# Kernel optimization log

Hardware: AMD Instinct MI355X
Metric: run time of the kernel (lower is better)

Reference implementation:

```python
import jax, jax.numpy as jnp
import numpy as np

LATENT = 64

def _linear(x, W, b):
    return x @ W.T + b

def setup_inputs() -> dict:
    key = jax.random.key(0)
    ks = jax.random.split(key, 16)
    B, D, H, L = 16384, 784, 1024, LATENT
    def u(k, shape, fan_in):
        bound = 1.0 / np.sqrt(fan_in)
        return jax.random.uniform(k, shape, jnp.float32, -bound, bound)
    inp = {
        "x": jax.random.uniform(ks[0], (B, D), jnp.float32),
        "epsilon": jax.random.normal(ks[1], (B, L), jnp.float32),
        "W_ih": u(ks[2], (H, D), D), "b_ih": u(ks[3], (H,), D),
        "W_m":  u(ks[4], (L, H), H), "b_m":  u(ks[5], (L,), H),
        "W_lv": u(ks[6], (L, H), H), "b_lv": u(ks[7], (L,), H),
        "W_ap": u(ks[8], (L, H), H), "b_ap": u(ks[9], (L,), H),
        "W_lh": u(ks[10], (H, L), L), "b_lh": u(ks[11], (H,), L),
        "W_ho": u(ks[12], (D, H), H), "b_ho": u(ks[13], (D,), H),
    }
    return inp

def reference(x, epsilon, W_ih, b_ih, W_m, b_m, W_lv, b_lv, W_ap, b_ap, W_lh, b_lh, W_ho, b_ho):
    # ----- encode -----
    hidden = jnp.tanh(_linear(x, W_ih, b_ih))            # [B,H]
    mean   = _linear(hidden, W_m, b_m)                   # [B,L]
    logvar = jnp.clip(_linear(hidden, W_lv, b_lv), -4.5, 0.0)  # Hardtanh(-4.5,0)
    approx = _linear(hidden, W_ap, b_ap)                 # [B,L]
    # ----- reparameterize (rank-1 Gaussian) -----
    # inv_cov = diag(exp(logvar)) + approx approx^T   per sample
    B, L = mean.shape
    eye = jnp.eye(L, dtype=mean.dtype)
    inv_cov = jnp.exp(logvar)[:, :, None] * eye + approx[:, :, None] * approx[:, None, :]  # [B,L,L]
    cov = jnp.linalg.inv(inv_cov)                        # batched 64x64 inverse
    # torch.potrf default returns UPPER Cholesky U with U^T U = cov -> U = chol(cov).T
    Sigma = jnp.swapaxes(jnp.linalg.cholesky(cov), -1, -2)  # [B,L,L] upper
    z = mean + jnp.einsum('bij,bj->bi', Sigma, epsilon)  # [B,L]
    # ----- decode -----
    h2 = jnp.tanh(_linear(z, W_lh, b_lh))
    x_mean = jax.nn.sigmoid(_linear(h2, W_ho, b_ho))     # [B,784]
    return (x_mean, z, mean, logvar, approx)
```

## Files before the change

kernel.cpp:

```cpp
#include <hip/hip_runtime.h>
#include <hip/hip_bf16.h>
#include <math.h>

typedef __attribute__((ext_vector_type(8))) short short8;
typedef __attribute__((ext_vector_type(4))) float f32x4;
typedef __attribute__((ext_vector_type(4))) unsigned short us4;

#define GLOBAL_AS __attribute__((address_space(1)))
#define LDS_AS __attribute__((address_space(3)))

__device__ inline void g2l16(const void* g, void* l) {
    __builtin_amdgcn_global_load_lds((const GLOBAL_AS void*)g, (LDS_AS void*)l, 16, 0, 0);
}

__device__ inline unsigned short f2bf(float f) {
    unsigned int u = __float_as_uint(f);
    return (unsigned short)((u + 0x7fffu + ((u >> 16) & 1u)) >> 16);
}

template <int EPI>
__global__ __launch_bounds__(512, 4) void mgemmB(
    const __hip_bfloat16* __restrict__ A,
    const __hip_bfloat16* __restrict__ W,
    const float* __restrict__ bias,
    void* __restrict__ outp,
    int lda, int ldb, int nT, int ldc, int Nreal)
{
    __shared__ __align__(16) __hip_bfloat16 sh[2][12288];

    const int tid  = threadIdx.x;
    const int wave = tid >> 6;
    const int lane = tid & 63;
    const int rBase = blockIdx.x * 256;
    const int cBase = blockIdx.y * 128;

    const __hip_bfloat16* Ab = A + (size_t)rBase * lda;
    const __hip_bfloat16* Wb = W + (size_t)cBase * ldb;

    const int wr = (wave >> 1) * 64;
    const int wc = (wave & 1) * 64;
    const int h  = lane >> 4;
    const int r0 = lane & 15;
    const int swz = h ^ ((r0 >> 1) & 3);

    f32x4 acc[4][4];
#pragma unroll
    for (int m = 0; m < 4; ++m)
#pragma unroll
        for (int n = 0; n < 4; ++n) acc[m][n] = (f32x4){0.f, 0.f, 0.f, 0.f};

    auto stage = [&](int bb, int t) {
        const int k0 = t * 32;
#pragma unroll
        for (int r = 0; r < 2; ++r) {
            int s2  = r * 512 + tid;
            int row = s2 >> 2;
            int cg  = (s2 & 3) ^ ((row >> 1) & 3);
            g2l16(Ab + (size_t)row * lda + k0 + cg * 8, &sh[bb][s2 * 8]);
        }
        {
            int s2  = tid;
            int row = s2 >> 2;
            int cg  = (s2 & 3) ^ ((row >> 1) & 3);
            g2l16(Wb + (size_t)row * ldb + k0 + cg * 8, &sh[bb][8192 + s2 * 8]);
        }
    };

    auto compute = [&](int bb) {
        const __hip_bfloat16* base = &sh[bb][0];
        short8 a_[4], b_[4];
#pragma unroll
        for (int m = 0; m < 4; ++m) {
            int R = wr + m * 16 + r0;
            a_[m] = *(const short8*)(base + (R * 4 + swz) * 8);
        }
#pragma unroll
        for (int n = 0; n < 4; ++n) {
            int R = wc + n * 16 + r0;
            b_[n] = *(const short8*)(base + 8192 + (R * 4 + swz) * 8);
        }
        __builtin_amdgcn_s_setprio(1);
#pragma unroll
        for (int m = 0; m < 4; ++m)
#pragma unroll
            for (int n = 0; n < 4; ++n)
                acc[m][n] = __builtin_amdgcn_mfma_f32_16x16x32_bf16(a_[m], b_[n], acc[m][n], 0, 0, 0);
        __builtin_amdgcn_s_setprio(0);
    };

    stage(0, 0);
    stage(1, 1);
    for (int t = 0; t < nT; ++t) {
        const int cur = t & 1;
        if (t + 1 < nT) asm volatile("s_waitcnt vmcnt(3)" ::: "memory");
        else            asm volatile("s_waitcnt vmcnt(0)" ::: "memory");
        __builtin_amdgcn_s_barrier();
        compute(cur);
        __builtin_amdgcn_s_barrier();
        if (t + 2 < nT) stage(cur, t + 2);
    }

    const int rq = lane >> 4;
    const int c0 = lane & 15;
#pragma unroll
    for (int m = 0; m < 4; ++m) {
#pragma unroll
        for (int n = 0; n < 4; ++n) {
            f32x4 v = acc[m][n];
            const int gc = cBase + wc + n * 16 + c0;
            const float bv = bias[gc];
#pragma unroll
            for (int j = 0; j < 4; ++j) {
                const int gr = rBase + wr + m * 16 + rq * 4 + j;
                float val = v[j] + bv;
                if (EPI == 1) {
                    ((__hip_bfloat16*)outp)[(size_t)gr * ldc + gc] = __float2bfloat16(tanhf(val));
                } else {
                    if (gc < Nreal)
                        ((float*)outp)[(size_t)gr * Nreal + gc] = 1.f / (1.f + expf(-val));
                }
            }
        }
    }
}

template <int EPI>
__global__ __launch_bounds__(256, 4) void mgemmC(
    const __hip_bfloat16* __restrict__ A,
    const __hip_bfloat16* __restrict__ W,
    const float* __restrict__ bias,
    void* __restrict__ outp,
    int lda, int ldb, int nT, int ldc, int Nreal)
{
    __shared__ __align__(16) __hip_bfloat16 sh[2][8192];

    const int tid  = threadIdx.x;
    const int wave = tid >> 6;
    const int lane = tid & 63;
    const int rBase = blockIdx.x * 128;
    const int cBase = blockIdx.y * 128;

    const __hip_bfloat16* Ab = A + (size_t)rBase * lda;
    const __hip_bfloat16* Wb = W + (size_t)cBase * ldb;

    const int wr = (wave >> 1) * 64;
    const int wc = (wave & 1) * 64;
    const int h  = lane >> 4;
    const int r0 = lane & 15;
    const int swz = h ^ ((r0 >> 1) & 3);

    f32x4 acc[4][4];
#pragma unroll
    for (int m = 0; m < 4; ++m)
#pragma unroll
        for (int n = 0; n < 4; ++n) acc[m][n] = (f32x4){0.f, 0.f, 0.f, 0.f};

    auto stage = [&](int bb, int t) {
        const int k0 = t * 32;
#pragma unroll
        for (int r = 0; r < 2; ++r) {
            int s2  = r * 256 + tid;
            int row = s2 >> 2;
            int cg  = (s2 & 3) ^ ((row >> 1) & 3);
            g2l16(Ab + (size_t)row * lda + k0 + cg * 8, &sh[bb][s2 * 8]);
            g2l16(Wb + (size_t)row * ldb + k0 + cg * 8, &sh[bb][4096 + s2 * 8]);
        }
    };

    auto compute = [&](int bb) {
        const __hip_bfloat16* base = &sh[bb][0];
        short8 a_[4], b_[4];
#pragma unroll
        for (int m = 0; m < 4; ++m) {
            int R = wr + m * 16 + r0;
            a_[m] = *(const short8*)(base + (R * 4 + swz) * 8);
        }
#pragma unroll
        for (int n = 0; n < 4; ++n) {
            int R = wc + n * 16 + r0;
            b_[n] = *(const short8*)(base + 4096 + (R * 4 + swz) * 8);
        }
        __builtin_amdgcn_s_setprio(1);
#pragma unroll
        for (int m = 0; m < 4; ++m)
#pragma unroll
            for (int n = 0; n < 4; ++n)
                acc[m][n] = __builtin_amdgcn_mfma_f32_16x16x32_bf16(a_[m], b_[n], acc[m][n], 0, 0, 0);
        __builtin_amdgcn_s_setprio(0);
    };

    stage(0, 0);
    stage(1, 1);
    for (int t = 0; t < nT; ++t) {
        const int cur = t & 1;
        if (t + 1 < nT) asm volatile("s_waitcnt vmcnt(4)" ::: "memory");
        else            asm volatile("s_waitcnt vmcnt(0)" ::: "memory");
        __builtin_amdgcn_s_barrier();
        compute(cur);
        __builtin_amdgcn_s_barrier();
        if (t + 2 < nT) stage(cur, t + 2);
    }

    const int rq = lane >> 4;
    const int c0 = lane & 15;
#pragma unroll
    for (int m = 0; m < 4; ++m) {
#pragma unroll
        for (int n = 0; n < 4; ++n) {
            f32x4 v = acc[m][n];
            const int gc = cBase + wc + n * 16 + c0;
            const float bv = bias[gc];
#pragma unroll
            for (int j = 0; j < 4; ++j) {
                const int gr = rBase + wr + m * 16 + rq * 4 + j;
                float val = v[j] + bv;
                if (EPI == 1) {
                    ((__hip_bfloat16*)outp)[(size_t)gr * ldc + gc] = __float2bfloat16(tanhf(val));
                }
            }
        }
    }
}

__global__ __launch_bounds__(256, 2) void headrep(
    const __hip_bfloat16* __restrict__ hidden,
    const __hip_bfloat16* __restrict__ Whead,
    const float* __restrict__ bhead,
    const float* __restrict__ eps,
    float* __restrict__ meanp, float* __restrict__ logvarp,
    float* __restrict__ approxp, float* __restrict__ zp,
    __hip_bfloat16* __restrict__ zb)
{
    __shared__ __align__(16) __hip_bfloat16 sh[2][16384];

    const int tid  = threadIdx.x;
    const int wave = tid >> 6;
    const int lane = tid & 63;
    const int rBase = blockIdx.x * 64;

    const __hip_bfloat16* Ab = hidden + (size_t)rBase * 1024;

    const int wnb = wave * 48;
    const int h  = lane >> 4;
    const int r0 = lane & 15;
    const int swz = h ^ ((r0 >> 1) & 3);

    f32x4 acc[4][3];
#pragma unroll
    for (int m = 0; m < 4; ++m)
#pragma unroll
        for (int n = 0; n < 3; ++n) acc[m][n] = (f32x4){0.f, 0.f, 0.f, 0.f};

    auto stage = [&](int bb, int t) {
#pragma unroll
        for (int ks = 0; ks < 2; ++ks) {
            const int k0 = t * 64 + ks * 32;
            {
                int s2 = tid, row = s2 >> 2;
                int cg = (s2 & 3) ^ ((row >> 1) & 3);
                g2l16(Ab + (size_t)row * 1024 + k0 + cg * 8, &sh[bb][(ks * 256 + s2) * 8]);
            }
#pragma unroll
            for (int r = 0; r < 3; ++r) {
                int s2 = r * 256 + tid, row = s2 >> 2;
                int cg = (s2 & 3) ^ ((row >> 1) & 3);
                g2l16(Whead + (size_t)row * 1024 + k0 + cg * 8,
                      &sh[bb][(512 + ks * 768 + s2) * 8]);
            }
        }
    };

    auto compute = [&](int bb) {
#pragma unroll
        for (int ks = 0; ks < 2; ++ks) {
            const __hip_bfloat16* base = &sh[bb][0];
            short8 a_[4], b_[3];
#pragma unroll
            for (int m = 0; m < 4; ++m) {
                int R = m * 16 + r0;
                a_[m] = *(const short8*)(base + ((ks * 256) + R * 4 + swz) * 8);
            }
#pragma unroll
            for (int n = 0; n < 3; ++n) {
                int R = wnb + n * 16 + r0;
                b_[n] = *(const short8*)(base + (512 + ks * 768 + R * 4 + swz) * 8);
            }
            __builtin_amdgcn_s_setprio(1);
#pragma unroll
            for (int m = 0; m < 4; ++m)
#pragma unroll
                for (int n = 0; n < 3; ++n)
                    acc[m][n] = __builtin_amdgcn_mfma_f32_16x16x32_bf16(a_[m], b_[n], acc[m][n], 0, 0, 0);
            __builtin_amdgcn_s_setprio(0);
        }
    };

    stage(0, 0);
    stage(1, 1);
    const int nT = 16;
    for (int t = 0; t < nT; ++t) {
        const int cur = t & 1;
        if (t + 1 < nT) asm volatile("s_waitcnt vmcnt(8)" ::: "memory");
        else            asm volatile("s_waitcnt vmcnt(0)" ::: "memory");
        __builtin_amdgcn_s_barrier();
        compute(cur);
        __builtin_amdgcn_s_barrier();
        if (t + 2 < nT) stage(cur, t + 2);
    }

    float* cs = (float*)&sh[0][0];
    const int rq = lane >> 4;
    const int c0 = lane & 15;
#pragma unroll
    for (int m = 0; m < 4; ++m)
#pragma unroll
        for (int n = 0; n < 3; ++n)
#pragma unroll
            for (int j = 0; j < 4; ++j)
                cs[(m * 16 + rq * 4 + j) * 200 + wnb + n * 16 + c0] = acc[m][n][j];
    __syncthreads();

    const float bm_  = bhead[lane];
    const float blv_ = bhead[64 + lane];
    const float bap_ = bhead[128 + lane];
#pragma unroll 4
    for (int r16 = 0; r16 < 16; ++r16) {
        const int row = wave * 16 + r16;
        const int gr  = rBase + row;
        const float mv = cs[row * 200 + lane] + bm_;
        float lv = cs[row * 200 + 64 + lane] + blv_;
        lv = fminf(fmaxf(lv, -4.5f), 0.f);
        const float ap = cs[row * 200 + 128 + lane] + bap_;
        const float ep = eps[(size_t)gr * 64 + lane];

        const float s  = expf(-lv);
        const float x1 = ap * ap * s;
        const float x2 = s * ap * ep;
        float R = x1, S = x2;
#pragma unroll
        for (int off = 1; off < 64; off <<= 1) {
            float r2 = __shfl_down(R, off, 64);
            float s2 = __shfl_down(S, off, 64);
            if (lane + off < 64) { R += r2; S += s2; }
        }
        const float Rexc  = R - x1;
        const float Sexc  = S - x2;
        const float inv1R = 1.f / (1.f + R);
        const float dL    = sqrtf(s * (1.f + Rexc) * inv1R);
        const float bj    = -s * ap * inv1R / dL;
        const float zv    = mv + dL * ep + bj * Sexc;

        const size_t idx = (size_t)gr * 64 + lane;
        meanp[idx]   = mv;
        logvarp[idx] = lv;
        approxp[idx] = ap;
        zp[idx]      = zv;
        zb[idx]      = __float2bfloat16(zv);
    }
}

__global__ void prep1(const float* __restrict__ x, const float* __restrict__ Wih,
                      const float* __restrict__ Wm, const float* __restrict__ Wlv,
                      const float* __restrict__ Wap, const float* __restrict__ bm,
                      const float* __restrict__ blv, const float* __restrict__ bap,
                      const float* __restrict__ Who, const float* __restrict__ Wlh,
                      const float* __restrict__ bho_src,
                      unsigned short* __restrict__ slab,
                      unsigned short* __restrict__ whead,
                      unsigned short* __restrict__ whob,
                      unsigned short* __restrict__ wlhb,
                      float* __restrict__ bhead, float* __restrict__ bho)
{
    const long SEG0 = 17408L * 200;
    const long SEG1 = SEG0 + 65536;
    const long SEG2 = SEG1 + 262144;
    const long SEG3 = SEG2 + 16384;
    const long SEG4 = SEG3 + 64;
    const long SEG5 = SEG4 + 256;
    long u = (long)blockIdx.x * 256 + threadIdx.x;
    if (u < SEG0) {
        long r = u / 200;
        int  c = (int)(u - r * 200) * 4;
        us4 o = (us4){0, 0, 0, 0};
        if (c < 784) {
            const float* src = (r < 16384) ? (x + r * 784) : (Wih + (r - 16384) * 784);
            float4 v = *(const float4*)(src + c);
            o.x = f2bf(v.x); o.y = f2bf(v.y); o.z = f2bf(v.z); o.w = f2bf(v.w);
        }
        *(us4*)(slab + r * 800 + c) = o;
    } else if (u < SEG1) {
        long t = u - SEG0;
        int r = (int)(t >> 8), c = (int)(t & 255) * 4;
        us4 o = (us4){0, 0, 0, 0};
        const float* src = nullptr;
        if (r < 64)       src = Wm + (size_t)r * 1024;
        else if (r < 128) src = Wlv + (size_t)(r - 64) * 1024;
        else if (r < 192) src = Wap + (size_t)(r - 128) * 1024;
        if (src) {
            float4 v = *(const float4*)(src + c);
            o.x = f2bf(v.x); o.y = f2bf(v.y); o.z = f2bf(v.z); o.w = f2bf(v.w);
        }
        *(us4*)(whead + (size_t)r * 1024 + c) = o;
    } else if (u < SEG2) {
        long t = u - SEG1;
        int r = (int)(t >> 8), c = (int)(t & 255) * 4;
        us4 o = (us4){0, 0, 0, 0};
        if (r < 784) {
            float4 v = *(const float4*)(Who + (size_t)r * 1024 + c);
            o.x = f2bf(v.x); o.y = f2bf(v.y); o.z = f2bf(v.z); o.w = f2bf(v.w);
        }
        *(us4*)(whob + (size_t)r * 1024 + c) = o;
    } else if (u < SEG3) {
        long t = u - SEG2;
        int r = (int)(t >> 4), c = (int)(t & 15) * 4;
        float4 v = *(const float4*)(Wlh + (size_t)r * 64 + c);
        us4 o;
        o.x = f2bf(v.x); o.y = f2bf(v.y); o.z = f2bf(v.z); o.w = f2bf(v.w);
        *(us4*)(wlhb + (size_t)r * 64 + c) = o;
    } else if (u < SEG4) {
        int base = (int)(u - SEG3) * 4;
#pragma unroll
        for (int k = 0; k < 4; ++k) {
            int p = base + k;
            float v = 0.f;
            if (p < 64)       v = bm[p];
            else if (p < 128) v = blv[p - 64];
            else if (p < 192) v = bap[p - 128];
            bhead[p] = v;
        }
    } else if (u < SEG5) {
        int base = (int)(u - SEG4) * 4;
#pragma unroll
        for (int k = 0; k < 4; ++k) {
            int p = base + k;
            bho[p] = (p < 784) ? bho_src[p] : 0.f;
        }
    }
}

extern "C" void kernel_launch(void* const* d_in, const int* in_sizes, int n_in,
                              void* d_out, int out_size, void* d_ws, size_t ws_size,
                              hipStream_t stream)
{
    const float* x    = (const float*)d_in[0];
    const float* eps  = (const float*)d_in[1];
    const float* W_ih = (const float*)d_in[2];
    const float* b_ih = (const float*)d_in[3];
    const float* W_m  = (const float*)d_in[4];
    const float* b_m  = (const float*)d_in[5];
    const float* W_lv = (const float*)d_in[6];
    const float* b_lv = (const float*)d_in[7];
    const float* W_ap = (const float*)d_in[8];
    const float* b_ap = (const float*)d_in[9];
    const float* W_lh = (const float*)d_in[10];
    const float* b_lh = (const float*)d_in[11];
    const float* W_ho = (const float*)d_in[12];
    const float* b_ho = (const float*)d_in[13];

    const int B = 16384;

    float* out    = (float*)d_out;
    float* x_mean = out;
    float* z      = out + (size_t)B * 784;
    float* mean   = z + (size_t)B * 64;
    float* logvar = mean + (size_t)B * 64;
    float* approx = logvar + (size_t)B * 64;

    char* ws = (char*)d_ws;
    __hip_bfloat16* hb    = (__hip_bfloat16*)(ws + 0);
    __hip_bfloat16* xb    = (__hip_bfloat16*)(ws + 33554432);
    __hip_bfloat16* wihb  = (__hip_bfloat16*)(ws + 33554432 + 16384L * 800 * 2);
    __hip_bfloat16* whead = (__hip_bfloat16*)(ws + 61407232);
    __hip_bfloat16* whob  = (__hip_bfloat16*)(ws + 61931520);
    __hip_bfloat16* wlhb  = (__hip_bfloat16*)(ws + 64028672);
    float*          bhead = (float*)(ws + 64159744);
    float*          bho   = (float*)(ws + 64160768);
    __hip_bfloat16* zb    = (__hip_bfloat16*)(ws + 33554432);
    __hip_bfloat16* h2b   = hb;

    {
        long total = 17408L * 200 + 65536 + 262144 + 16384 + 64 + 256;
        prep1<<<dim3((total + 255) / 256), dim3(256), 0, stream>>>(
            x, W_ih, W_m, W_lv, W_ap, b_m, b_lv, b_ap, W_ho, W_lh, b_ho,
            (unsigned short*)xb, (unsigned short*)whead, (unsigned short*)whob,
            (unsigned short*)wlhb, bhead, bho);
    }

    mgemmB<1><<<dim3(64, 8), dim3(512), 0, stream>>>(xb, wihb, b_ih, hb, 800, 800, 25, 1024, 1024);

    headrep<<<dim3(256), dim3(256), 0, stream>>>(hb, whead, bhead, eps,
                                                 mean, logvar, approx, z, zb);

    mgemmC<1><<<dim3(128, 8), dim3(256), 0, stream>>>(zb, wlhb, b_lh, h2b, 64, 64, 2, 1024, 1024);

    mgemmB<2><<<dim3(64, 7), dim3(512), 0, stream>>>(h2b, whob, bho, x_mean, 1024, 1024, 32, 784, 784);
}
```

Baseline: 144.9 us.

## Fuse latent-to-hidden decoder GEMM into head/reparameterization kernel

```diff
diff --git a/kernel.cpp b/kernel.cpp
--- a/kernel.cpp
+++ b/kernel.cpp
@@ -124,112 +124,16 @@
     }
 }
 
-template <int EPI>
-__global__ __launch_bounds__(256, 4) void mgemmC(
-    const __hip_bfloat16* __restrict__ A,
-    const __hip_bfloat16* __restrict__ W,
-    const float* __restrict__ bias,
-    void* __restrict__ outp,
-    int lda, int ldb, int nT, int ldc, int Nreal)
-{
-    __shared__ __align__(16) __hip_bfloat16 sh[2][8192];
-
-    const int tid  = threadIdx.x;
-    const int wave = tid >> 6;
-    const int lane = tid & 63;
-    const int rBase = blockIdx.x * 128;
-    const int cBase = blockIdx.y * 128;
-
-    const __hip_bfloat16* Ab = A + (size_t)rBase * lda;
-    const __hip_bfloat16* Wb = W + (size_t)cBase * ldb;
-
-    const int wr = (wave >> 1) * 64;
-    const int wc = (wave & 1) * 64;
-    const int h  = lane >> 4;
-    const int r0 = lane & 15;
-    const int swz = h ^ ((r0 >> 1) & 3);
-
-    f32x4 acc[4][4];
-#pragma unroll
-    for (int m = 0; m < 4; ++m)
-#pragma unroll
-        for (int n = 0; n < 4; ++n) acc[m][n] = (f32x4){0.f, 0.f, 0.f, 0.f};
-
-    auto stage = [&](int bb, int t) {
-        const int k0 = t * 32;
-#pragma unroll
-        for (int r = 0; r < 2; ++r) {
-            int s2  = r * 256 + tid;
-            int row = s2 >> 2;
-            int cg  = (s2 & 3) ^ ((row >> 1) & 3);
-            g2l16(Ab + (size_t)row * lda + k0 + cg * 8, &sh[bb][s2 * 8]);
-            g2l16(Wb + (size_t)row * ldb + k0 + cg * 8, &sh[bb][4096 + s2 * 8]);
-        }
-    };
-
-    auto compute = [&](int bb) {
-        const __hip_bfloat16* base = &sh[bb][0];
-        short8 a_[4], b_[4];
-#pragma unroll
-        for (int m = 0; m < 4; ++m) {
-            int R = wr + m * 16 + r0;
-            a_[m] = *(const short8*)(base + (R * 4 + swz) * 8);
-        }
-#pragma unroll
-        for (int n = 0; n < 4; ++n) {
-            int R = wc + n * 16 + r0;
-            b_[n] = *(const short8*)(base + 4096 + (R * 4 + swz) * 8);
-        }
-        __builtin_amdgcn_s_setprio(1);
-#pragma unroll
-        for (int m = 0; m < 4; ++m)
-#pragma unroll
-            for (int n = 0; n < 4; ++n)
-                acc[m][n] = __builtin_amdgcn_mfma_f32_16x16x32_bf16(a_[m], b_[n], acc[m][n], 0, 0, 0);
-        __builtin_amdgcn_s_setprio(0);
-    };
-
-    stage(0, 0);
-    stage(1, 1);
-    for (int t = 0; t < nT; ++t) {
-        const int cur = t & 1;
-        if (t + 1 < nT) asm volatile("s_waitcnt vmcnt(4)" ::: "memory");
-        else            asm volatile("s_waitcnt vmcnt(0)" ::: "memory");
-        __builtin_amdgcn_s_barrier();
-        compute(cur);
-        __builtin_amdgcn_s_barrier();
-        if (t + 2 < nT) stage(cur, t + 2);
-    }
-
-    const int rq = lane >> 4;
-    const int c0 = lane & 15;
-#pragma unroll
-    for (int m = 0; m < 4; ++m) {
-#pragma unroll
-        for (int n = 0; n < 4; ++n) {
-            f32x4 v = acc[m][n];
-            const int gc = cBase + wc + n * 16 + c0;
-            const float bv = bias[gc];
-#pragma unroll
-            for (int j = 0; j < 4; ++j) {
-                const int gr = rBase + wr + m * 16 + rq * 4 + j;
-                float val = v[j] + bv;
-                if (EPI == 1) {
-                    ((__hip_bfloat16*)outp)[(size_t)gr * ldc + gc] = __float2bfloat16(tanhf(val));
-                }
-            }
-        }
-    }
-}
-
 __global__ __launch_bounds__(256, 2) void headrep(
     const __hip_bfloat16* __restrict__ hidden,
     const __hip_bfloat16* __restrict__ Whead,
+    const __hip_bfloat16* __restrict__ Wlh,
     const float* __restrict__ bhead,
+    const float* __restrict__ blh,
     const float* __restrict__ eps,
     float* __restrict__ meanp, float* __restrict__ logvarp,
     float* __restrict__ approxp, float* __restrict__ zp,
-    __hip_bfloat16* __restrict__ zb)
+    __hip_bfloat16* __restrict__ h2out)
 {
     __shared__ __align__(16) __hip_bfloat16 sh[2][16384];
 
@@ -309,6 +213,7 @@
     }
 
     float* cs = (float*)&sh[0][0];
+    __hip_bfloat16* zs = (__hip_bfloat16*)((char*)&sh[0][0] + 52224);
     const int rq = lane >> 4;
     const int c0 = lane & 15;
 #pragma unroll
@@ -355,7 +260,50 @@
         logvarp[idx] = lv;
         approxp[idx] = ap;
         zp[idx]      = zv;
-        zb[idx]      = __float2bfloat16(zv);
+        zs[row * 80 + lane] = __float2bfloat16(zv);
+    }
+    __syncthreads();
+
+#pragma unroll
+    for (int nc = 0; nc < 4; ++nc) {
+        const int cb = wave * 256 + nc * 64;
+        f32x4 acc2[4][4];
+#pragma unroll
+        for (int m = 0; m < 4; ++m)
+#pragma unroll
+            for (int n = 0; n < 4; ++n) acc2[m][n] = (f32x4){0.f, 0.f, 0.f, 0.f};
+#pragma unroll
+        for (int ks = 0; ks < 2; ++ks) {
+            short8 a2[4], b2[4];
+#pragma unroll
+            for (int m = 0; m < 4; ++m) {
+                int R = m * 16 + r0;
+                a2[m] = *(const short8*)(zs + R * 80 + ks * 32 + h * 8);
+            }
+#pragma unroll
+            for (int n = 0; n < 4; ++n) {
+                int R = cb + n * 16 + r0;
+                b2[n] = *(const short8*)(Wlh + (size_t)R * 64 + ks * 32 + h * 8);
+            }
+#pragma unroll
+            for (int m = 0; m < 4; ++m)
+#pragma unroll
+                for (int n = 0; n < 4; ++n)
+                    acc2[m][n] = __builtin_amdgcn_mfma_f32_16x16x32_bf16(a2[m], b2[n], acc2[m][n], 0, 0, 0);
+        }
+#pragma unroll
+        for (int m = 0; m < 4; ++m) {
+#pragma unroll
+            for (int n = 0; n < 4; ++n) {
+                const int gc = cb + n * 16 + c0;
+                const float bv = blh[gc];
+#pragma unroll
+                for (int j = 0; j < 4; ++j) {
+                    const int gr = rBase + m * 16 + rq * 4 + j;
+                    h2out[(size_t)gr * 1024 + gc] = __float2bfloat16(tanhf(acc2[m][n][j] + bv));
+                }
+            }
+        }
     }
 }
 
@@ -475,8 +423,6 @@
     __hip_bfloat16* wlhb  = (__hip_bfloat16*)(ws + 64028672);
     float*          bhead = (float*)(ws + 64159744);
     float*          bho   = (float*)(ws + 64160768);
-    __hip_bfloat16* zb    = (__hip_bfloat16*)(ws + 33554432);
-    __hip_bfloat16* h2b   = hb;
 
     {
         long total = 17408L * 200 + 65536 + 262144 + 16384 + 64 + 256;
@@ -488,10 +434,8 @@
 
     mgemmB<1><<<dim3(64, 8), dim3(512), 0, stream>>>(xb, wihb, b_ih, hb, 800, 800, 25, 1024, 1024);
 
-    headrep<<<dim3(256), dim3(256), 0, stream>>>(hb, whead, bhead, eps,
-                                                 mean, logvar, approx, z, zb);
-
-    mgemmC<1><<<dim3(128, 8), dim3(256), 0, stream>>>(zb, wlhb, b_lh, h2b, 64, 64, 2, 1024, 1024);
-
-    mgemmB<2><<<dim3(64, 7), dim3(512), 0, stream>>>(h2b, whob, bho, x_mean, 1024, 1024, 32, 784, 784);
-}
+    headrep<<<dim3(256), dim3(256), 0, stream>>>(hb, whead, wlhb, bhead, b_lh, eps,
+                                                 mean, logvar, approx, z, hb);
+
+    mgemmB<2><<<dim3(64, 7), dim3(512), 0, stream>>>(hb, whob, bho, x_mean, 1024, 1024, 32, 784, 784);
+}
```

Measured after the change: 158.8 us. +9.6%, slower.
